# Kernel tuning notes

Hardware: AMD Instinct MI355X
Metric: run time of the kernel (lower is better)

## Reference

```python
import jax, jax.numpy as jnp
import numpy as np

B, T = 64, 256
V, E, H, TAGS = 50000, 256, 512, 50


def setup_inputs() -> dict:
    key = jax.random.key(0)
    ks = jax.random.split(key, 20)
    x = jax.random.randint(ks[0], (B, T), 0, V, dtype=jnp.int64)
    lengths = jax.random.randint(ks[1], (B,), 1, T + 1, dtype=jnp.int64)
    lengths = lengths.at[0].set(T)  # pad_packed width == T
    s = 0.05
    def w(k, shape):
        return jax.random.normal(k, shape, dtype=jnp.float32) * s
    inp = {"x": x, "lengths": lengths, "emb": w(ks[2], (V, E))}
    # layer1: input E, layer2: input 2H; gate order i,f,g,o (PyTorch).
    # single bias per direction == b_ih + b_hh combined.
    names = [("f1", E), ("b1", E), ("f2", 2 * H), ("b2", 2 * H)]
    ki = 3
    for name, din in names:
        inp["w_ih_" + name] = w(ks[ki], (4 * H, din)); ki += 1
        inp["w_hh_" + name] = w(ks[ki], (4 * H, H)); ki += 1
        inp["b_" + name] = w(ks[ki], (4 * H,)); ki += 1
    inp["cls_w"] = w(ks[ki], (TAGS, 2 * H)); ki += 1
    inp["cls_b"] = w(ks[ki], (TAGS,))
    return inp


def _reverse_padded(x, lengths):
    # per-row reversal of the first `lengths[b]` steps; padding stays zero
    Tn = x.shape[1]
    idx = lengths[:, None] - 1 - jnp.arange(Tn)[None, :]  # [B,T]
    valid = idx >= 0
    idx = jnp.clip(idx, 0)
    out = jnp.take_along_axis(x, idx[:, :, None], axis=1)
    return jnp.where(valid[:, :, None], out, 0.0)


def _lstm_scan(x_pre, lengths, w_hh):
    # x_pre: [B,T,4H] = x @ w_ih.T + b ; masked LSTM over time
    Bn, Tn, H4 = x_pre.shape
    Hn = H4 // 4
    h0 = jnp.zeros((Bn, Hn), x_pre.dtype)
    c0 = jnp.zeros((Bn, Hn), x_pre.dtype)

    def step(carry, inp):
        h, c = carry
        pre_t, t = inp
        gates = pre_t + h @ w_hh.T
        i, f, g, o = jnp.split(gates, 4, axis=-1)
        i = jax.nn.sigmoid(i); f = jax.nn.sigmoid(f)
        g = jnp.tanh(g); o = jax.nn.sigmoid(o)
        c_new = f * c + i * g
        h_new = o * jnp.tanh(c_new)
        m = (t < lengths)[:, None]
        h = jnp.where(m, h_new, h)
        c = jnp.where(m, c_new, c)
        out = jnp.where(m, h_new, 0.0)
        return (h, c), out

    xs = (jnp.swapaxes(x_pre, 0, 1), jnp.arange(Tn))
    _, ys = jax.lax.scan(step, (h0, c0), xs)
    return jnp.swapaxes(ys, 0, 1)  # [B,T,H]


def _bilstm(x, lengths, w_ih_f, w_hh_f, b_f, w_ih_b, w_hh_b, b_b):
    out_f = _lstm_scan(x @ w_ih_f.T + b_f, lengths, w_hh_f)
    xr = _reverse_padded(x, lengths)
    out_b = _lstm_scan(xr @ w_ih_b.T + b_b, lengths, w_hh_b)
    out_b = _reverse_padded(out_b, lengths)
    return jnp.concatenate([out_f, out_b], axis=-1)


def reference(x, lengths, emb, w_ih_f1, w_hh_f1, b_f1, w_ih_b1, w_hh_b1, b_b1,
              w_ih_f2, w_hh_f2, b_f2, w_ih_b2, w_hh_b2, b_b2, cls_w, cls_b):
    e = emb[x]  # [B,T,E]
    out1 = _bilstm(e, lengths, w_ih_f1, w_hh_f1, b_f1, w_ih_b1, w_hh_b1, b_b1)
    out2 = _bilstm(out1, lengths, w_ih_f2, w_hh_f2, b_f2, w_ih_b2, w_hh_b2, b_b2)
    # dropout is identity at eval time
    logits = out2 @ cls_w.T + cls_b  # [B,T,TAGS]
    return logits
```

## Files before the change

kernel.cpp:

```cpp
#include <hip/hip_runtime.h>
#include <hip/hip_bf16.h>

#define BB 64
#define TT 256
#define HH 512
#define EE 256
#define NTAGS 50
#define BT (BB * TT)

typedef _Float16 f16;
typedef __attribute__((ext_vector_type(2))) _Float16 half2v;
typedef __attribute__((ext_vector_type(4))) _Float16 half4;
typedef __attribute__((ext_vector_type(8))) _Float16 half8;
typedef __attribute__((ext_vector_type(8))) short short8;
typedef __attribute__((ext_vector_type(4))) float f32x4;
typedef __hip_bfloat16 bf16;

__device__ __forceinline__ float sigm(float x) {
    return 1.f / (1.f + __expf(-x));
}
__device__ __forceinline__ float tanh_f(float x) {
    float ax = fabsf(x);
    float e = __expf(2.f * ax);
    float t = 1.f - 2.f / (e + 1.f);
    return x < 0.f ? -t : t;
}
__device__ __forceinline__ short f2bs(float f) {
    return (short)__bfloat16_as_ushort(__float2bfloat16(f));
}
__device__ __forceinline__ void split8v(const float* vv, bf16* hi, bf16* lo) {
    short8 h8, l8;
#pragma unroll
    for (int j = 0; j < 8; ++j) {
        bf16 h = __float2bfloat16(vv[j]);
        h8[j] = (short)__bfloat16_as_ushort(h);
        l8[j] = f2bs(vv[j] - __bfloat162float(h));
    }
    *(short8*)hi = h8;
    *(short8*)lo = l8;
}
__device__ __forceinline__ void split8(const float* p, bf16* hi, bf16* lo) {
    float4 v0 = *(const float4*)p;
    float4 v1 = *(const float4*)(p + 4);
    float vv[8] = {v0.x, v0.y, v0.z, v0.w, v1.x, v1.y, v1.z, v1.w};
    split8v(vv, hi, lo);
}
__device__ __forceinline__ void split8h(const f16* p, bf16* hi, bf16* lo) {
    half8 a = *(const half8*)p;
    float vv[8];
#pragma unroll
    for (int j = 0; j < 8; ++j) vv[j] = (float)a[j];
    split8v(vv, hi, lo);
}
__device__ __forceinline__ void cvt8h(const f16* p, bf16* hi) {
    half8 a = *(const half8*)p;
    short8 h8;
#pragma unroll
    for (int j = 0; j < 8; ++j)
        h8[j] = (short)__bfloat16_as_ushort(__float2bfloat16((float)a[j]));
    *(short8*)hi = h8;
}

__global__ void bar_init(int* __restrict__ bar) {
    bar[blockIdx.x * 256 + threadIdx.x] = 0;
}

__global__ __launch_bounds__(256) void gemm_emb(
    const int* __restrict__ x, const float* __restrict__ emb,
    const float* __restrict__ W, const float* __restrict__ bias,
    f16* __restrict__ C) {
    __shared__ bf16 Ah[128][72], Al[128][72];
    __shared__ bf16 Wh[128][72], Wl[128][72];
    const int m0 = blockIdx.x * 128;
    const int n0 = blockIdx.y * 128;
    const int tid = threadIdx.x;
    const int wave = tid >> 6;
    const int lane = tid & 63;
    const int lrow = lane & 15;
    const int quad = lane >> 4;
    const int msub = (wave >> 1) * 64;
    const int nsub = (wave & 1) * 64;

    int tok[4];
#pragma unroll
    for (int c = 0; c < 4; ++c)
        tok[c] = x[m0 + ((c * 256 + tid) >> 3)];

    f32x4 acc[4][4];
#pragma unroll
    for (int i = 0; i < 4; ++i)
#pragma unroll
        for (int j = 0; j < 4; ++j) acc[i][j] = (f32x4){0.f, 0.f, 0.f, 0.f};

    for (int k0 = 0; k0 < EE; k0 += 64) {
        __syncthreads();
#pragma unroll
        for (int c = 0; c < 4; ++c) {
            int f = c * 256 + tid;
            int row = f >> 3;
            int kc = f & 7;
            split8(emb + (size_t)tok[c] * EE + k0 + kc * 8,
                   &Ah[row][kc * 8], &Al[row][kc * 8]);
            split8(W + (size_t)(n0 + row) * EE + k0 + kc * 8,
                   &Wh[row][kc * 8], &Wl[row][kc * 8]);
        }
        __syncthreads();
#pragma unroll
        for (int ks = 0; ks < 2; ++ks) {
            short8 ah[4], al[4], bh[4], bl[4];
#pragma unroll
            for (int i = 0; i < 4; ++i) {
                ah[i] = *(const short8*)&Ah[msub + i * 16 + lrow][ks * 32 + quad * 8];
                al[i] = *(const short8*)&Al[msub + i * 16 + lrow][ks * 32 + quad * 8];
            }
#pragma unroll
            for (int j = 0; j < 4; ++j) {
                bh[j] = *(const short8*)&Wh[nsub + j * 16 + lrow][ks * 32 + quad * 8];
                bl[j] = *(const short8*)&Wl[nsub + j * 16 + lrow][ks * 32 + quad * 8];
            }
#pragma unroll
            for (int i = 0; i < 4; ++i)
#pragma unroll
                for (int j = 0; j < 4; ++j) {
                    acc[i][j] = __builtin_amdgcn_mfma_f32_16x16x32_bf16(ah[i], bh[j], acc[i][j], 0, 0, 0);
                    acc[i][j] = __builtin_amdgcn_mfma_f32_16x16x32_bf16(ah[i], bl[j], acc[i][j], 0, 0, 0);
                    acc[i][j] = __builtin_amdgcn_mfma_f32_16x16x32_bf16(al[i], bh[j], acc[i][j], 0, 0, 0);
                }
        }
    }

#pragma unroll
    for (int j = 0; j < 4; ++j) {
        int n = n0 + nsub + j * 16 + lrow;
        float bv = bias[n];
#pragma unroll
        for (int i = 0; i < 4; ++i)
#pragma unroll
            for (int r = 0; r < 4; ++r) {
                int m = m0 + msub + i * 16 + quad * 4 + r;
                C[(size_t)m * 2048 + n] = (f16)(acc[i][j][r] + bv);
            }
    }
}

__global__ __launch_bounds__(256) void gemm_l2(
    const f16* __restrict__ A, const float* __restrict__ W,
    const float* __restrict__ bias, f16* __restrict__ C) {
    __shared__ bf16 Ah[128][72];
    __shared__ bf16 Wh[128][72], Wl[128][72];
    const int m0 = blockIdx.x * 128;
    const int n0 = blockIdx.y * 128;
    const int tid = threadIdx.x;
    const int wave = tid >> 6;
    const int lane = tid & 63;
    const int lrow = lane & 15;
    const int quad = lane >> 4;
    const int msub = (wave >> 1) * 64;
    const int nsub = (wave & 1) * 64;

    f32x4 acc[4][4];
#pragma unroll
    for (int i = 0; i < 4; ++i)
#pragma unroll
        for (int j = 0; j < 4; ++j) acc[i][j] = (f32x4){0.f, 0.f, 0.f, 0.f};

    for (int k0 = 0; k0 < 1024; k0 += 64) {
        __syncthreads();
#pragma unroll
        for (int c = 0; c < 4; ++c) {
            int f = c * 256 + tid;
            int row = f >> 3;
            int kc = f & 7;
            cvt8h(A + (size_t)(m0 + row) * 1024 + k0 + kc * 8, &Ah[row][kc * 8]);
            split8(W + (size_t)(n0 + row) * 1024 + k0 + kc * 8,
                   &Wh[row][kc * 8], &Wl[row][kc * 8]);
        }
        __syncthreads();
#pragma unroll
        for (int ks = 0; ks < 2; ++ks) {
            short8 ah[4], bh[4], bl[4];
#pragma unroll
            for (int i = 0; i < 4; ++i)
                ah[i] = *(const short8*)&Ah[msub + i * 16 + lrow][ks * 32 + quad * 8];
#pragma unroll
            for (int j = 0; j < 4; ++j) {
                bh[j] = *(const short8*)&Wh[nsub + j * 16 + lrow][ks * 32 + quad * 8];
                bl[j] = *(const short8*)&Wl[nsub + j * 16 + lrow][ks * 32 + quad * 8];
            }
#pragma unroll
            for (int i = 0; i < 4; ++i)
#pragma unroll
                for (int j = 0; j < 4; ++j) {
                    acc[i][j] = __builtin_amdgcn_mfma_f32_16x16x32_bf16(ah[i], bh[j], acc[i][j], 0, 0, 0);
                    acc[i][j] = __builtin_amdgcn_mfma_f32_16x16x32_bf16(ah[i], bl[j], acc[i][j], 0, 0, 0);
                }
        }
    }

#pragma unroll
    for (int j = 0; j < 4; ++j) {
        int n = n0 + nsub + j * 16 + lrow;
        float bv = bias[n];
#pragma unroll
        for (int i = 0; i < 4; ++i)
#pragma unroll
            for (int r = 0; r < 4; ++r) {
                int m = m0 + msub + i * 16 + quad * 4 + r;
                C[(size_t)m * 2048 + n] = (f16)(acc[i][j][r] + bv);
            }
    }
}

__global__ __launch_bounds__(256) void cls_gemm(
    const f16* __restrict__ A, const float* __restrict__ W,
    const float* __restrict__ bias, float* __restrict__ C) {
    __shared__ bf16 Ah[128][72], Al[128][72];
    __shared__ bf16 Wh[64][72], Wl[64][72];
    const int m0 = blockIdx.x * 128;
    const int tid = threadIdx.x;
    const int wave = tid >> 6;
    const int lane = tid & 63;
    const int lrow = lane & 15;
    const int quad = lane >> 4;
    const int msub = wave * 32;

    f32x4 acc[2][4];
#pragma unroll
    for (int i = 0; i < 2; ++i)
#pragma unroll
        for (int j = 0; j < 4; ++j) acc[i][j] = (f32x4){0.f, 0.f, 0.f, 0.f};

    for (int k0 = 0; k0 < 1024; k0 += 64) {
        __syncthreads();
#pragma unroll
        for (int c = 0; c < 4; ++c) {
            int f = c * 256 + tid;
            int row = f >> 3;
            int kc = f & 7;
            split8h(A + (size_t)(m0 + row) * 1024 + k0 + kc * 8,
                    &Ah[row][kc * 8], &Al[row][kc * 8]);
        }
#pragma unroll
        for (int c = 0; c < 2; ++c) {
            int f = c * 256 + tid;
            int row = f >> 3;
            int kc = f & 7;
            int wr = row < NTAGS ? row : NTAGS - 1;
            split8(W + (size_t)wr * 1024 + k0 + kc * 8,
                   &Wh[row][kc * 8], &Wl[row][kc * 8]);
        }
        __syncthreads();
#pragma unroll
        for (int ks = 0; ks < 2; ++ks) {
            short8 ah[2], al[2], bh[4], bl[4];
#pragma unroll
            for (int i = 0; i < 2; ++i) {
                ah[i] = *(const short8*)&Ah[msub + i * 16 + lrow][ks * 32 + quad * 8];
                al[i] = *(const short8*)&Al[msub + i * 16 + lrow][ks * 32 + quad * 8];
            }
#pragma unroll
            for (int j = 0; j < 4; ++j) {
                bh[j] = *(const short8*)&Wh[j * 16 + lrow][ks * 32 + quad * 8];
                bl[j] = *(const short8*)&Wl[j * 16 + lrow][ks * 32 + quad * 8];
            }
#pragma unroll
            for (int i = 0; i < 2; ++i)
#pragma unroll
                for (int j = 0; j < 4; ++j) {
                    acc[i][j] = __builtin_amdgcn_mfma_f32_16x16x32_bf16(ah[i], bh[j], acc[i][j], 0, 0, 0);
                    acc[i][j] = __builtin_amdgcn_mfma_f32_16x16x32_bf16(ah[i], bl[j], acc[i][j], 0, 0, 0);
                    acc[i][j] = __builtin_amdgcn_mfma_f32_16x16x32_bf16(al[i], bh[j], acc[i][j], 0, 0, 0);
                }
        }
    }

#pragma unroll
    for (int j = 0; j < 4; ++j) {
        int n = j * 16 + lrow;
        if (n < NTAGS) {
            float bv = bias[n];
#pragma unroll
            for (int i = 0; i < 2; ++i)
#pragma unroll
                for (int r = 0; r < 4; ++r) {
                    int m = m0 + msub + i * 16 + quad * 4 + r;
                    C[(size_t)m * NTAGS + n] = acc[i][j][r] + bv;
                }
        }
    }
}

__global__ __launch_bounds__(256, 1) void lstm_scan(
    const f16* __restrict__ xpre_f, const f16* __restrict__ xpre_b,
    const float* __restrict__ whh_f, const float* __restrict__ whh_b,
    const int* __restrict__ lengths,
    f16* __restrict__ out,
    bf16* __restrict__ hbuf,
    int* __restrict__ bar, int base) {
    __shared__ bf16 w_lo2[32][64][8];
    __shared__ float gat[64][33];
    __shared__ int len_s[64];

    const int dir = blockIdx.x >> 6;
    const int sl = blockIdx.x & 63;
    const int tid = threadIdx.x;
    const int wave = tid >> 6;
    const int lane = tid & 63;
    const int lrow = lane & 15;
    const int quad = lane >> 4;
    const int gb = wave * 16 + (lane >> 2);
    const int up = lane & 3;
    const int u0 = up * 2;

    const f16* xpre = dir ? xpre_b : xpre_f;
    const float* whh = dir ? whh_b : whh_f;
    bf16* hb = hbuf + (size_t)dir * 2 * 2 * BB * HH;
    int* flags = bar + dir * 8192;
    int* myflag = flags + (wave * 64 + sl) * 16;
    int* pollp = flags + (wave * 64 + lane) * 16;

    short8 BH[2][16];
#pragma unroll
    for (int nt = 0; nt < 2; ++nt) {
        int R = nt * 16 + lrow;
        const float* wr = whh + (size_t)((R >> 3) * HH + sl * 8 + (R & 7)) * HH + quad * 8;
#pragma unroll
        for (int c = 0; c < 16; ++c) {
            float4 v0 = *(const float4*)(wr + c * 32);
            float4 v1 = *(const float4*)(wr + c * 32 + 4);
            float vv[8] = {v0.x, v0.y, v0.z, v0.w, v1.x, v1.y, v1.z, v1.w};
            short8 h8, l8;
#pragma unroll
            for (int j = 0; j < 8; ++j) {
                bf16 h = __float2bfloat16(vv[j]);
                h8[j] = (short)__bfloat16_as_ushort(h);
                l8[j] = f2bs(vv[j] - __bfloat162float(h));
            }
            BH[nt][c] = h8;
            *(short8*)&w_lo2[nt * 16 + c][lane][0] = l8;
        }
    }
    if (tid < 64) len_s[tid] = lengths[tid];
    __syncthreads();

    float hr0 = 0.f, hr1 = 0.f, cr0 = 0.f, cr1 = 0.f;

    float pr[2][4];
    {
        int len = len_s[gb];
        int ta = dir ? (len - 1) : 0;
        const f16* xp = xpre + (size_t)(gb * TT + ta) * 2048 + sl * 8 + u0;
        half2v g0 = *(const half2v*)(xp);
        half2v g1 = *(const half2v*)(xp + 512);
        half2v g2 = *(const half2v*)(xp + 1024);
        half2v g3 = *(const half2v*)(xp + 1536);
        pr[0][0] = (float)g0[0]; pr[1][0] = (float)g0[1];
        pr[0][1] = (float)g1[0]; pr[1][1] = (float)g1[1];
        pr[0][2] = (float)g2[0]; pr[1][2] = (float)g2[1];
        pr[0][3] = (float)g3[0]; pr[1][3] = (float)g3[1];
    }

    for (int s = 0; s < TT; ++s) {
        if (s > 0) {
            const int target = base + s;

            {
                int v = __hip_atomic_load(pollp, __ATOMIC_RELAXED,
                                          __HIP_MEMORY_SCOPE_AGENT);
                while (__ballot(v >= target) != ~0ull) {
                    __builtin_amdgcn_s_sleep(1);
                    v = __hip_atomic_load(pollp, __ATOMIC_RELAXED,
                                          __HIP_MEMORY_SCOPE_AGENT);
                }
            }
            __asm__ volatile("" ::: "memory");

            const int b = wave * 16 + lrow;
            const char* hpb = (const char*)hb +
                (size_t)(((s & 1) ^ 1) * 2) * BB * HH * sizeof(bf16);
            const char* hib = hpb + b * 1024 + quad * 16;

            short8 AH[16];
#pragma unroll
            for (int c = 0; c < 16; ++c) {
                asm volatile("global_load_dwordx4 %0, %1, off offset:%2 sc0 sc1"
                             : "=v"(AH[c]) : "v"(hib), "n"(c * 64));
            }

            f32x4 ac[2][2];
            ac[0][0] = (f32x4){0.f, 0.f, 0.f, 0.f};
            ac[0][1] = (f32x4){0.f, 0.f, 0.f, 0.f};
            ac[1][0] = (f32x4){0.f, 0.f, 0.f, 0.f};
            ac[1][1] = (f32x4){0.f, 0.f, 0.f, 0.f};

            asm volatile("s_waitcnt vmcnt(8)" ::: "memory");
            __builtin_amdgcn_sched_barrier(0);
#pragma unroll
            for (int c = 0; c < 8; ++c) {
#pragma unroll
                for (int nt = 0; nt < 2; ++nt) {
                    short8 bll = *(const short8*)&w_lo2[nt * 16 + c][lane][0];
                    ac[nt][c & 1] = __builtin_amdgcn_mfma_f32_16x16x32_bf16(AH[c], BH[nt][c], ac[nt][c & 1], 0, 0, 0);
                    ac[nt][c & 1] = __builtin_amdgcn_mfma_f32_16x16x32_bf16(AH[c], bll, ac[nt][c & 1], 0, 0, 0);
                }
            }
            asm volatile("s_waitcnt vmcnt(0)" ::: "memory");
            __builtin_amdgcn_sched_barrier(0);
#pragma unroll
            for (int c = 8; c < 16; ++c) {
#pragma unroll
                for (int nt = 0; nt < 2; ++nt) {
                    short8 bll = *(const short8*)&w_lo2[nt * 16 + c][lane][0];
                    ac[nt][c & 1] = __builtin_amdgcn_mfma_f32_16x16x32_bf16(AH[c], BH[nt][c], ac[nt][c & 1], 0, 0, 0);
                    ac[nt][c & 1] = __builtin_amdgcn_mfma_f32_16x16x32_bf16(AH[c], bll, ac[nt][c & 1], 0, 0, 0);
                }
            }
#pragma unroll
            for (int nt = 0; nt < 2; ++nt)
#pragma unroll
                for (int r = 0; r < 4; ++r)
                    gat[wave * 16 + quad * 4 + r][nt * 16 + lrow] =
                        ac[nt][0][r] + ac[nt][1][r];
            asm volatile("s_waitcnt lgkmcnt(0)" ::: "memory");
            __builtin_amdgcn_sched_barrier(0);
        }

        const int len = len_s[gb];
        const bool act = (s < len);
        if (act) {
            float z0[4], z1[4];
#pragma unroll
            for (int g = 0; g < 4; ++g) { z0[g] = pr[0][g]; z1[g] = pr[1][g]; }
            if (s > 0) {
#pragma unroll
                for (int g = 0; g < 4; ++g) {
                    z0[g] += gat[gb][g * 8 + u0];
                    z1[g] += gat[gb][g * 8 + u0 + 1];
                }
            }
            float i0 = sigm(z0[0]), f0 = sigm(z0[1]);
            float g0 = tanh_f(z0[2]), o0 = sigm(z0[3]);
            float i1 = sigm(z1[0]), f1 = sigm(z1[1]);
            float g1 = tanh_f(z1[2]), o1 = sigm(z1[3]);
            cr0 = f0 * cr0 + i0 * g0;
            cr1 = f1 * cr1 + i1 * g1;
            hr0 = o0 * tanh_f(cr0);
            hr1 = o1 * tanh_f(cr1);
        }
        {
            bf16 bh0 = __float2bfloat16(hr0);
            bf16 bh1 = __float2bfloat16(hr1);
            unsigned int hw = (unsigned int)__bfloat16_as_ushort(bh0) |
                              ((unsigned int)__bfloat16_as_ushort(bh1) << 16);
            char* hcb = (char*)hb + (size_t)((s & 1) * 2) * BB * HH * sizeof(bf16);
            char* pa = hcb + gb * 1024 + (sl * 8 + u0) * 2;
            asm volatile("global_store_dword %0, %1, off sc0 sc1"
                         :: "v"(pa), "v"(hw) : "memory");
        }
        asm volatile("s_waitcnt vmcnt(0)" ::: "memory");
        if (lane == 0)
            __hip_atomic_store(myflag, base + s + 1, __ATOMIC_RELAXED,
                               __HIP_MEMORY_SCOPE_AGENT);

        if (s + 1 < TT) {
            if (s + 1 < len) {
                int ta = dir ? (len - 2 - s) : (s + 1);
                const f16* xp = xpre + (size_t)(gb * TT + ta) * 2048 + sl * 8 + u0;
                half2v g0 = *(const half2v*)(xp);
                half2v g1 = *(const half2v*)(xp + 512);
                half2v g2 = *(const half2v*)(xp + 1024);
                half2v g3 = *(const half2v*)(xp + 1536);
                pr[0][0] = (float)g0[0]; pr[1][0] = (float)g0[1];
                pr[0][1] = (float)g1[0]; pr[1][1] = (float)g1[1];
                pr[0][2] = (float)g2[0]; pr[1][2] = (float)g2[1];
                pr[0][3] = (float)g3[0]; pr[1][3] = (float)g3[1];
            }
        }
        if (act) {
            int ta = dir ? (len - 1 - s) : s;
            half2v ov; ov[0] = (f16)hr0; ov[1] = (f16)hr1;
            *(half2v*)(out + (size_t)(gb * TT + ta) * 1024 + dir * 512 + sl * 8 + u0) = ov;
        } else {
            half2v zv; zv[0] = (f16)0.f; zv[1] = (f16)0.f;
            *(half2v*)(out + (size_t)(gb * TT + s) * 1024 + dir * 512 + sl * 8 + u0) = zv;
        }
    }
}

extern "C" void kernel_launch(void* const* d_in, const int* in_sizes, int n_in,
                              void* d_out, int out_size, void* d_ws, size_t ws_size,
                              hipStream_t stream) {
    const int* x = (const int*)d_in[0];
    const int* lengths = (const int*)d_in[1];
    const float* emb = (const float*)d_in[2];
    const float* w_ih_f1 = (const float*)d_in[3];
    const float* w_hh_f1 = (const float*)d_in[4];
    const float* b_f1 = (const float*)d_in[5];
    const float* w_ih_b1 = (const float*)d_in[6];
    const float* w_hh_b1 = (const float*)d_in[7];
    const float* b_b1 = (const float*)d_in[8];
    const float* w_ih_f2 = (const float*)d_in[9];
    const float* w_hh_f2 = (const float*)d_in[10];
    const float* b_f2 = (const float*)d_in[11];
    const float* w_ih_b2 = (const float*)d_in[12];
    const float* w_hh_b2 = (const float*)d_in[13];
    const float* b_b2 = (const float*)d_in[14];
    const float* cls_w = (const float*)d_in[15];
    const float* cls_b = (const float*)d_in[16];
    float* logits = (float*)d_out;

    char* ws = (char*)d_ws;
    int* bar = (int*)ws;
    bf16* hbuf = (bf16*)(ws + 65536);
    f16* xpre_f = (f16*)(ws + 16777216);
    f16* xpre_b = (f16*)(ws + 83886080);
    f16* out1 = (f16*)(ws + 150994944);
    f16* out2 = out1;

    bar_init<<<64, 256, 0, stream>>>(bar);

    dim3 g1(BT / 128, 2048 / 128);
    gemm_emb<<<g1, 256, 0, stream>>>(x, emb, w_ih_f1, b_f1, xpre_f);
    gemm_emb<<<g1, 256, 0, stream>>>(x, emb, w_ih_b1, b_b1, xpre_b);
    lstm_scan<<<128, 256, 0, stream>>>(xpre_f, xpre_b, w_hh_f1, w_hh_b1,
                                       lengths, out1, hbuf, bar, 0);

    gemm_l2<<<g1, 256, 0, stream>>>(out1, w_ih_f2, b_f2, xpre_f);
    gemm_l2<<<g1, 256, 0, stream>>>(out1, w_ih_b2, b_b2, xpre_b);
    lstm_scan<<<128, 256, 0, stream>>>(xpre_f, xpre_b, w_hh_f2, w_hh_b2,
                                       lengths, out2, hbuf, bar, TT);

    cls_gemm<<<BT / 128, 256, 0, stream>>>(out2, cls_w, cls_b, logits);
}
```

Measured before the change: 2.677 ms.

## Skip padded row tiles in GEMMs and split recurrent MFMA waits finer

The input-projection and classifier GEMMs now return early for 128-row tiles that lie entirely beyond a sequence's length. In the classifier those tiles are filled with the bias directly, which matches the reference because padded outputs are zero. The recurrent step issues its hidden-state loads in four groups with staged vmcnt waits, and four accumulator chains instead of two, so MFMAs can start sooner and dependency chains are shorter. The cost is a few extra accumulator registers plus a per-block length check.

```diff
diff --git a/kernel.cpp b/kernel.cpp
--- a/kernel.cpp
+++ b/kernel.cpp
@@ -68,10 +68,12 @@
 __global__ __launch_bounds__(256) void gemm_emb(
     const int* __restrict__ x, const float* __restrict__ emb,
     const float* __restrict__ W, const float* __restrict__ bias,
-    f16* __restrict__ C) {
+    const int* __restrict__ lengths, f16* __restrict__ C) {
+    const int m0 = blockIdx.x * 128;
+    if ((m0 & 255) >= lengths[m0 >> 8]) return;
+
     __shared__ bf16 Ah[128][72], Al[128][72];
     __shared__ bf16 Wh[128][72], Wl[128][72];
-    const int m0 = blockIdx.x * 128;
     const int n0 = blockIdx.y * 128;
     const int tid = threadIdx.x;
     const int wave = tid >> 6;
@@ -145,10 +147,13 @@
 
 __global__ __launch_bounds__(256) void gemm_l2(
     const f16* __restrict__ A, const float* __restrict__ W,
-    const float* __restrict__ bias, f16* __restrict__ C) {
+    const float* __restrict__ bias, const int* __restrict__ lengths,
+    f16* __restrict__ C) {
+    const int m0 = blockIdx.x * 128;
+    if ((m0 & 255) >= lengths[m0 >> 8]) return;
+
     __shared__ bf16 Ah[128][72];
     __shared__ bf16 Wh[128][72], Wl[128][72];
-    const int m0 = blockIdx.x * 128;
     const int n0 = blockIdx.y * 128;
     const int tid = threadIdx.x;
     const int wave = tid >> 6;
@@ -213,11 +218,20 @@
 
 __global__ __launch_bounds__(256) void cls_gemm(
     const f16* __restrict__ A, const float* __restrict__ W,
-    const float* __restrict__ bias, float* __restrict__ C) {
+    const float* __restrict__ bias, const int* __restrict__ lengths,
+    float* __restrict__ C) {
+    const int m0 = blockIdx.x * 128;
+    const int tid = threadIdx.x;
+    if ((m0 & 255) >= lengths[m0 >> 8]) {
+        for (int f = tid; f < 128 * NTAGS; f += 256) {
+            int r = f / NTAGS, n = f % NTAGS;
+            C[(size_t)(m0 + r) * NTAGS + n] = bias[n];
+        }
+        return;
+    }
+
     __shared__ bf16 Ah[128][72], Al[128][72];
     __shared__ bf16 Wh[64][72], Wl[64][72];
-    const int m0 = blockIdx.x * 128;
-    const int tid = threadIdx.x;
     const int wave = tid >> 6;
     const int lane = tid & 63;
     const int lrow = lane & 15;
@@ -387,40 +401,59 @@
                              : "=v"(AH[c]) : "v"(hib), "n"(c * 64));
             }
 
-            f32x4 ac[2][2];
-            ac[0][0] = (f32x4){0.f, 0.f, 0.f, 0.f};
-            ac[0][1] = (f32x4){0.f, 0.f, 0.f, 0.f};
-            ac[1][0] = (f32x4){0.f, 0.f, 0.f, 0.f};
-            ac[1][1] = (f32x4){0.f, 0.f, 0.f, 0.f};
-
+            f32x4 ac[2][4];
+#pragma unroll
+            for (int nt = 0; nt < 2; ++nt)
+#pragma unroll
+                for (int q = 0; q < 4; ++q)
+                    ac[nt][q] = (f32x4){0.f, 0.f, 0.f, 0.f};
+
+            asm volatile("s_waitcnt vmcnt(12)" ::: "memory");
+            __builtin_amdgcn_sched_barrier(0);
+#pragma unroll
+            for (int c = 0; c < 4; ++c)
+#pragma unroll
+                for (int nt = 0; nt < 2; ++nt) {
+                    short8 bll = *(const short8*)&w_lo2[nt * 16 + c][lane][0];
+                    ac[nt][c & 3] = __builtin_amdgcn_mfma_f32_16x16x32_bf16(AH[c], BH[nt][c], ac[nt][c & 3], 0, 0, 0);
+                    ac[nt][c & 3] = __builtin_amdgcn_mfma_f32_16x16x32_bf16(AH[c], bll, ac[nt][c & 3], 0, 0, 0);
+                }
             asm volatile("s_waitcnt vmcnt(8)" ::: "memory");
             __builtin_amdgcn_sched_barrier(0);
 #pragma unroll
-            for (int c = 0; c < 8; ++c) {
+            for (int c = 4; c < 8; ++c)
 #pragma unroll
                 for (int nt = 0; nt < 2; ++nt) {
                     short8 bll = *(const short8*)&w_lo2[nt * 16 + c][lane][0];
-                    ac[nt][c & 1] = __builtin_amdgcn_mfma_f32_16x16x32_bf16(AH[c], BH[nt][c], ac[nt][c & 1], 0, 0, 0);
-                    ac[nt][c & 1] = __builtin_amdgcn_mfma_f32_16x16x32_bf16(AH[c], bll, ac[nt][c & 1], 0, 0, 0);
-                }
-            }
+                    ac[nt][c & 3] = __builtin_amdgcn_mfma_f32_16x16x32_bf16(AH[c], BH[nt][c], ac[nt][c & 3], 0, 0, 0);
+                    ac[nt][c & 3] = __builtin_amdgcn_mfma_f32_16x16x32_bf16(AH[c], bll, ac[nt][c & 3], 0, 0, 0);
+                }
+            asm volatile("s_waitcnt vmcnt(4)" ::: "memory");
+            __builtin_amdgcn_sched_barrier(0);
+#pragma unroll
+            for (int c = 8; c < 12; ++c)
+#pragma unroll
+                for (int nt = 0; nt < 2; ++nt) {
+                    short8 bll = *(const short8*)&w_lo2[nt * 16 + c][lane][0];
+                    ac[nt][c & 3] = __builtin_amdgcn_mfma_f32_16x16x32_bf16(AH[c], BH[nt][c], ac[nt][c & 3], 0, 0, 0);
+                    ac[nt][c & 3] = __builtin_amdgcn_mfma_f32_16x16x32_bf16(AH[c], bll, ac[nt][c & 3], 0, 0, 0);
+                }
             asm volatile("s_waitcnt vmcnt(0)" ::: "memory");
             __builtin_amdgcn_sched_barrier(0);
 #pragma unroll
-            for (int c = 8; c < 16; ++c) {
+            for (int c = 12; c < 16; ++c)
 #pragma unroll
                 for (int nt = 0; nt < 2; ++nt) {
                     short8 bll = *(const short8*)&w_lo2[nt * 16 + c][lane][0];
-                    ac[nt][c & 1] = __builtin_amdgcn_mfma_f32_16x16x32_bf16(AH[c], BH[nt][c], ac[nt][c & 1], 0, 0, 0);
-                    ac[nt][c & 1] = __builtin_amdgcn_mfma_f32_16x16x32_bf16(AH[c], bll, ac[nt][c & 1], 0, 0, 0);
-                }
-            }
+                    ac[nt][c & 3] = __builtin_amdgcn_mfma_f32_16x16x32_bf16(AH[c], BH[nt][c], ac[nt][c & 3], 0, 0, 0);
+                    ac[nt][c & 3] = __builtin_amdgcn_mfma_f32_16x16x32_bf16(AH[c], bll, ac[nt][c & 3], 0, 0, 0);
+                }
 #pragma unroll
             for (int nt = 0; nt < 2; ++nt)
 #pragma unroll
                 for (int r = 0; r < 4; ++r)
                     gat[wave * 16 + quad * 4 + r][nt * 16 + lrow] =
-                        ac[nt][0][r] + ac[nt][1][r];
+                        (ac[nt][0][r] + ac[nt][1][r]) + (ac[nt][2][r] + ac[nt][3][r]);
             asm volatile("s_waitcnt lgkmcnt(0)" ::: "memory");
             __builtin_amdgcn_sched_barrier(0);
         }
@@ -520,15 +553,15 @@
     bar_init<<<64, 256, 0, stream>>>(bar);
 
     dim3 g1(BT / 128, 2048 / 128);
-    gemm_emb<<<g1, 256, 0, stream>>>(x, emb, w_ih_f1, b_f1, xpre_f);
-    gemm_emb<<<g1, 256, 0, stream>>>(x, emb, w_ih_b1, b_b1, xpre_b);
+    gemm_emb<<<g1, 256, 0, stream>>>(x, emb, w_ih_f1, b_f1, lengths, xpre_f);
+    gemm_emb<<<g1, 256, 0, stream>>>(x, emb, w_ih_b1, b_b1, lengths, xpre_b);
     lstm_scan<<<128, 256, 0, stream>>>(xpre_f, xpre_b, w_hh_f1, w_hh_b1,
                                        lengths, out1, hbuf, bar, 0);
 
-    gemm_l2<<<g1, 256, 0, stream>>>(out1, w_ih_f2, b_f2, xpre_f);
-    gemm_l2<<<g1, 256, 0, stream>>>(out1, w_ih_b2, b_b2, xpre_b);
+    gemm_l2<<<g1, 256, 0, stream>>>(out1, w_ih_f2, b_f2, lengths, xpre_f);
+    gemm_l2<<<g1, 256, 0, stream>>>(out1, w_ih_b2, b_b2, lengths, xpre_b);
     lstm_scan<<<128, 256, 0, stream>>>(xpre_f, xpre_b, w_hh_f2, w_hh_b2,
                                        lengths, out2, hbuf, bar, TT);
 
-    cls_gemm<<<BT / 128, 256, 0, stream>>>(out2, cls_w, cls_b, logits);
-}
+    cls_gemm<<<BT / 128, 256, 0, stream>>>(out2, cls_w, cls_b, lengths, logits);
+}
```

After: 2.564 ms. 4.2% less time.
